# Optimization experiments

Measured on AMD Instinct MI355X. Metric: run time of the kernel, lower is better.

## Reference

```python
import jax, jax.numpy as jnp
import numpy as np

B, N, M, C = 64, 16384, 128, 1024  # batch, memory slots, memory unit size, ctrl dim
EPS = 1e-16


def _linear_params(k, fan_in, fan_out, gain=1.4):
    k1, k2 = jax.random.split(k)
    bound = gain * np.sqrt(6.0 / (fan_in + fan_out))  # xavier_uniform
    w = jax.random.uniform(k1, (fan_in, fan_out), jnp.float32, -bound, bound)
    b = jax.random.normal(k2, (fan_out,), jnp.float32) * 0.01
    return w, b


def setup_inputs() -> dict:
    key = jax.random.key(0)
    ks = jax.random.split(key, 10)
    ctrl_state = jax.random.normal(ks[0], (B, C), jnp.float32)
    pw = jax.random.uniform(ks[1], (B, N), jnp.float32)
    prev_weights = pw / pw.sum(axis=1, keepdims=True)
    memory = jax.random.normal(ks[2], (B, N, M), jnp.float32)
    key_w, key_b = _linear_params(ks[3], C, M)
    beta_w, beta_b = _linear_params(ks[4], C, 1)
    gate_w, gate_b = _linear_params(ks[5], C, 1)
    shift_w, shift_b = _linear_params(ks[6], C, 3)
    gamma_w, gamma_b = _linear_params(ks[7], C, 1)
    erase_w, erase_b = _linear_params(ks[8], C, M)
    add_w, add_b = _linear_params(ks[9], C, M)
    return dict(ctrl_state=ctrl_state, prev_weights=prev_weights, memory=memory,
                key_w=key_w, key_b=key_b, beta_w=beta_w, beta_b=beta_b,
                gate_w=gate_w, gate_b=gate_b, shift_w=shift_w, shift_b=shift_b,
                gamma_w=gamma_w, gamma_b=gamma_b, erase_w=erase_w, erase_b=erase_b,
                add_w=add_w, add_b=add_b)


def reference(ctrl_state, prev_weights, memory,
              key_w, key_b, beta_w, beta_b, gate_w, gate_b,
              shift_w, shift_b, gamma_w, gamma_b,
              erase_w, erase_b, add_w, add_b):
    # ---- parameter projections (7 small GEMMs + activations) ----
    k = jnp.tanh(ctrl_state @ key_w + key_b)                      # (B, M)
    beta = jax.nn.softplus(ctrl_state @ beta_w + beta_b)          # (B, 1)
    gate = jax.nn.sigmoid(ctrl_state @ gate_w + gate_b)           # (B, 1)
    shift = jax.nn.softmax(ctrl_state @ shift_w + shift_b, axis=1)  # (B, 3)
    gamma = 1.0 + jax.nn.softplus(ctrl_state @ gamma_w + gamma_b)   # (B, 1)
    # erase/add are computed by the head but unused in read ('r') mode
    _erase = jax.nn.sigmoid(ctrl_state @ erase_w + erase_b)
    _add = jnp.tanh(ctrl_state @ add_w + add_b)
    # ---- content addressing: cosine similarity then beta-sharpened softmax ----
    dots = jnp.einsum('bm,bnm->bn', k, memory)                    # (B, N)
    norms = jnp.linalg.norm(k, axis=1, keepdims=True) * jnp.linalg.norm(memory, axis=2)
    sim = dots / (norms + EPS)
    content_weights = jax.nn.softmax(beta * sim, axis=1)          # (B, N)
    # ---- gated interpolation ----
    w = gate * content_weights + (1.0 - gate) * prev_weights      # (B, N)
    # ---- circular convolutional shift (3-tap, max_shift=1) ----
    w = (shift[:, 0:1] * jnp.roll(w, 1, axis=1)
         + shift[:, 1:2] * w
         + shift[:, 2:3] * jnp.roll(w, -1, axis=1))
    # ---- sharpen ----
    wp = w ** gamma
    weights = wp / (wp.sum(axis=1, keepdims=True) + EPS)          # (B, N)
    # ---- read ----
    read_vec = jnp.einsum('bn,bnm->bm', weights, memory)          # (B, M)
    return weights, read_vec
```

## Files before the change

### kernel.cpp

```cpp
#include <hip/hip_runtime.h>
#include <math.h>

#define B_ 64
#define N_ 16384
#define M_ 128
#define C_ 1024
#define EPS_ 1e-16f

__device__ __forceinline__ float softplus_(float x) {
    return fmaxf(x, 0.f) + log1pf(expf(-fabsf(x)));
}

__global__ void proj_kernel(const float* __restrict__ ctrl,
                            const float* __restrict__ key_w, const float* __restrict__ key_b,
                            const float* __restrict__ beta_w, const float* __restrict__ beta_b,
                            const float* __restrict__ gate_w, const float* __restrict__ gate_b,
                            const float* __restrict__ shift_w, const float* __restrict__ shift_b,
                            const float* __restrict__ gamma_w, const float* __restrict__ gamma_b,
                            float* __restrict__ k_out, float* __restrict__ kn_out,
                            float* __restrict__ beta_out, float* __restrict__ gate_out,
                            float* __restrict__ gamma_out, float* __restrict__ shift_out)
{
    const int b = blockIdx.x;
    const int t = threadIdx.x;
    const float* c = ctrl + (size_t)b * C_;

    float acc = 0.f;
    for (int i = 0; i < C_; ++i) acc = fmaf(c[i], key_w[i * M_ + t], acc);
    float kv = tanhf(acc + key_b[t]);
    k_out[b * M_ + t] = kv;

    float p0 = 0, p1 = 0, p2 = 0, p3 = 0, p4 = 0, p5 = 0;
    for (int i = t; i < C_; i += 128) {
        float cv = c[i];
        p0 = fmaf(cv, beta_w[i],      p0);
        p1 = fmaf(cv, gate_w[i],      p1);
        p2 = fmaf(cv, gamma_w[i],     p2);
        p3 = fmaf(cv, shift_w[3*i+0], p3);
        p4 = fmaf(cv, shift_w[3*i+1], p4);
        p5 = fmaf(cv, shift_w[3*i+2], p5);
    }
    __shared__ float red[7][128];
    red[0][t] = p0; red[1][t] = p1; red[2][t] = p2;
    red[3][t] = p3; red[4][t] = p4; red[5][t] = p5;
    red[6][t] = kv * kv;
    __syncthreads();
    for (int s = 64; s > 0; s >>= 1) {
        if (t < s) {
            #pragma unroll
            for (int j = 0; j < 7; ++j) red[j][t] += red[j][t + s];
        }
        __syncthreads();
    }
    if (t == 0) {
        beta_out[b]  = softplus_(red[0][0] + beta_b[0]);
        gate_out[b]  = 1.f / (1.f + expf(-(red[1][0] + gate_b[0])));
        gamma_out[b] = 1.f + softplus_(red[2][0] + gamma_b[0]);
        float z0 = red[3][0] + shift_b[0];
        float z1 = red[4][0] + shift_b[1];
        float z2 = red[5][0] + shift_b[2];
        float mx = fmaxf(z0, fmaxf(z1, z2));
        float e0 = expf(z0 - mx), e1 = expf(z1 - mx), e2 = expf(z2 - mx);
        float inv = 1.f / (e0 + e1 + e2);
        shift_out[b*3+0] = e0 * inv;
        shift_out[b*3+1] = e1 * inv;
        shift_out[b*3+2] = e2 * inv;
        kn_out[b] = sqrtf(red[6][0]);
    }
}

#define ROWS_PER_CHUNK 1024
__global__ void content_kernel(const float* __restrict__ mem,
                               const float* __restrict__ k,
                               const float* __restrict__ kn,
                               const float* __restrict__ beta,
                               float* __restrict__ e_out,
                               float* __restrict__ sumE)
{
    const int b     = blockIdx.y;
    const int chunk = blockIdx.x;
    const int t     = threadIdx.x;
    const int wave  = t >> 6;
    const int lane  = t & 63;
    const int half  = lane >> 5;
    const int sub   = lane & 31;

    __shared__ float ks[M_];
    if (t < M_) ks[t] = k[b * M_ + t];
    __syncthreads();
    const float4 k4  = reinterpret_cast<const float4*>(ks)[sub];
    const float  knb = kn[b];
    const float  bet = beta[b];

    const float* memb = mem + (size_t)b * N_ * M_;
    const int rowbase = chunk * ROWS_PER_CHUNK + wave * 2 + half;

    float eacc = 0.f;
    #pragma unroll 4
    for (int i = 0; i < ROWS_PER_CHUNK / 8; ++i) {
        const int n = rowbase + i * 8;
        const float4 m4 = reinterpret_cast<const float4*>(memb + (size_t)n * M_)[sub];
        float d = m4.x*k4.x + m4.y*k4.y + m4.z*k4.z + m4.w*k4.w;
        float q = m4.x*m4.x + m4.y*m4.y + m4.z*m4.z + m4.w*m4.w;
        #pragma unroll
        for (int off = 1; off < 32; off <<= 1) {
            d += __shfl_xor(d, off, 64);
            q += __shfl_xor(q, off, 64);
        }
        if (sub == 0) {
            float sim = d / (knb * sqrtf(q) + EPS_);
            float ev  = expf(bet * sim);
            e_out[(size_t)b * N_ + n] = ev;
            eacc += ev;
        }
    }
    __shared__ float red[256];
    red[t] = eacc;
    __syncthreads();
    for (int s = 128; s > 0; s >>= 1) {
        if (t < s) red[t] += red[t + s];
        __syncthreads();
    }
    if (t == 0) atomicAdd(&sumE[b], red[0]);
}

__global__ void shiftpow_kernel(const float* __restrict__ e,
                                const float* __restrict__ prev,
                                const float* __restrict__ sumE,
                                const float* __restrict__ gate,
                                const float* __restrict__ shift,
                                const float* __restrict__ gamma,
                                float* __restrict__ wp_out,
                                float* __restrict__ sumWp)
{
    const int b = blockIdx.y;
    const int n = blockIdx.x * 256 + threadIdx.x;
    const float invE = 1.f / sumE[b];
    const float g    = gate[b];
    const float s0   = shift[b*3+0], s1 = shift[b*3+1], s2 = shift[b*3+2];
    const float gam  = gamma[b];
    const float* eb = e    + (size_t)b * N_;
    const float* pb = prev + (size_t)b * N_;

    const int nm = (n == 0)      ? N_ - 1 : n - 1;
    const int np = (n == N_ - 1) ? 0      : n + 1;
    float wm = g * eb[nm] * invE + (1.f - g) * pb[nm];
    float wc = g * eb[n]  * invE + (1.f - g) * pb[n];
    float wq = g * eb[np] * invE + (1.f - g) * pb[np];
    float wsft = s0 * wm + s1 * wc + s2 * wq;
    float wp = powf(wsft, gam);
    wp_out[(size_t)b * N_ + n] = wp;

    __shared__ float red[256];
    red[threadIdx.x] = wp;
    __syncthreads();
    for (int s = 128; s > 0; s >>= 1) {
        if (threadIdx.x < s) red[threadIdx.x] += red[threadIdx.x + s];
        __syncthreads();
    }
    if (threadIdx.x == 0) atomicAdd(&sumWp[b], red[0]);
}

__global__ void normalize_kernel(const float* __restrict__ wp,
                                 const float* __restrict__ sumWp,
                                 float* __restrict__ out_w)
{
    const int b = blockIdx.y;
    const int i = blockIdx.x * 256 + threadIdx.x;
    const float inv = 1.f / (sumWp[b] + EPS_);
    float4 v = reinterpret_cast<const float4*>(wp + (size_t)b * N_)[i];
    v.x *= inv; v.y *= inv; v.z *= inv; v.w *= inv;
    reinterpret_cast<float4*>(out_w + (size_t)b * N_)[i] = v;
}

__global__ void read_kernel(const float* __restrict__ mem,
                            const float* __restrict__ weights,
                            float* __restrict__ read_out)
{
    const int b     = blockIdx.y;
    const int chunk = blockIdx.x;
    const int t     = threadIdx.x;
    const int wave  = t >> 6;
    const int lane  = t & 63;
    const int half  = lane >> 5;
    const int sub   = lane & 31;

    __shared__ float wtile[ROWS_PER_CHUNK];
    for (int i = t; i < ROWS_PER_CHUNK; i += 256)
        wtile[i] = weights[(size_t)b * N_ + chunk * ROWS_PER_CHUNK + i];
    __syncthreads();

    const float* memb = mem + (size_t)b * N_ * M_;
    const int rowbase = chunk * ROWS_PER_CHUNK + wave * 2 + half;
    const int lbase   = wave * 2 + half;

    float4 acc = make_float4(0.f, 0.f, 0.f, 0.f);
    #pragma unroll 4
    for (int i = 0; i < ROWS_PER_CHUNK / 8; ++i) {
        const int n  = rowbase + i * 8;
        const float wn = wtile[lbase + i * 8];
        const float4 m4 = reinterpret_cast<const float4*>(memb + (size_t)n * M_)[sub];
        acc.x = fmaf(wn, m4.x, acc.x);
        acc.y = fmaf(wn, m4.y, acc.y);
        acc.z = fmaf(wn, m4.z, acc.z);
        acc.w = fmaf(wn, m4.w, acc.w);
    }
    __shared__ float red[8][32][4];
    const int g = wave * 2 + half;
    red[g][sub][0] = acc.x; red[g][sub][1] = acc.y;
    red[g][sub][2] = acc.z; red[g][sub][3] = acc.w;
    __syncthreads();
    if (t < M_) {
        const int m = t, s2 = m >> 2, c = m & 3;
        float s = 0.f;
        #pragma unroll
        for (int gg = 0; gg < 8; ++gg) s += red[gg][s2][c];
        atomicAdd(&read_out[b * M_ + m], s);
    }
}

extern "C" void kernel_launch(void* const* d_in, const int* in_sizes, int n_in,
                              void* d_out, int out_size, void* d_ws, size_t ws_size,
                              hipStream_t stream) {
    const float* ctrl    = (const float*)d_in[0];
    const float* prev_w  = (const float*)d_in[1];
    const float* memory  = (const float*)d_in[2];
    const float* key_w   = (const float*)d_in[3];
    const float* key_b   = (const float*)d_in[4];
    const float* beta_w  = (const float*)d_in[5];
    const float* beta_b  = (const float*)d_in[6];
    const float* gate_w  = (const float*)d_in[7];
    const float* gate_b  = (const float*)d_in[8];
    const float* shift_w = (const float*)d_in[9];
    const float* shift_b = (const float*)d_in[10];
    const float* gamma_w = (const float*)d_in[11];
    const float* gamma_b = (const float*)d_in[12];

    float* out   = (float*)d_out;
    float* ws    = (float*)d_ws;
    float* e     = ws;
    float* wp    = ws + (size_t)B_ * N_;
    float* kbuf  = ws + (size_t)2 * B_ * N_;
    float* kn    = kbuf  + B_ * M_;
    float* beta  = kn    + B_;
    float* gate  = beta  + B_;
    float* gamma = gate  + B_;
    float* shift = gamma + B_;
    float* sums  = shift + 3 * B_;
    float* sumE  = sums;
    float* sumWp = sums + B_;

    hipMemsetAsync(sums, 0, 2 * B_ * sizeof(float), stream);
    hipMemsetAsync(out + (size_t)B_ * N_, 0, B_ * M_ * sizeof(float), stream);

    proj_kernel<<<B_, 128, 0, stream>>>(ctrl, key_w, key_b, beta_w, beta_b,
                                        gate_w, gate_b, shift_w, shift_b,
                                        gamma_w, gamma_b,
                                        kbuf, kn, beta, gate, gamma, shift);

    content_kernel<<<dim3(N_ / ROWS_PER_CHUNK, B_), 256, 0, stream>>>(
        memory, kbuf, kn, beta, e, sumE);

    shiftpow_kernel<<<dim3(N_ / 256, B_), 256, 0, stream>>>(
        e, prev_w, sumE, gate, shift, gamma, wp, sumWp);

    normalize_kernel<<<dim3(N_ / 4 / 256, B_), 256, 0, stream>>>(wp, sumWp, out);

    read_kernel<<<dim3(N_ / ROWS_PER_CHUNK, B_), 256, 0, stream>>>(
        memory, out, out + (size_t)B_ * N_);
}
```

Baseline: 901.5 us.

## Fuse normalization into read kernel, widen proj block, restructure content row reduction

The normalize kernel is removed: the read kernel now scales the unnormalized powered weights by the inverse sum while loading its tile, and writes the normalized weights out. The content kernel assigns 8 lanes per memory row, each holding four float4s, so the cross-lane reduction drops from five shuffle steps to three. The projection kernel uses 256 threads and splits the key GEMM reduction across two halves. These changes aim to cut one launch and one full pass over the weights, and to reduce shuffle overhead in the bandwidth-bound content pass, at the cost of more registers per lane.

Result: slower. 1.034 ms (+14.7%).

```diff
diff --git a/kernel.cpp b/kernel.cpp
--- a/kernel.cpp
+++ b/kernel.cpp
@@ -6,6 +6,7 @@
 #define M_ 128
 #define C_ 1024
 #define EPS_ 1e-16f
+#define CHUNK_ 1024
 
 __device__ __forceinline__ float softplus_(float x) {
     return fmaxf(x, 0.f) + log1pf(expf(-fabsf(x)));
@@ -25,13 +26,24 @@
     const int t = threadIdx.x;
     const float* c = ctrl + (size_t)b * C_;
 
+    const int m    = t & 127;
+    const int half = t >> 7;
     float acc = 0.f;
-    for (int i = 0; i < C_; ++i) acc = fmaf(c[i], key_w[i * M_ + t], acc);
-    float kv = tanhf(acc + key_b[t]);
-    k_out[b * M_ + t] = kv;
+    const int i0 = half * (C_ / 2);
+    for (int i = i0; i < i0 + C_ / 2; ++i)
+        acc = fmaf(c[i], key_w[i * M_ + m], acc);
+
+    __shared__ float kred[256];
+    kred[t] = acc;
+    __syncthreads();
+    float kv = 0.f;
+    if (t < 128) {
+        kv = tanhf(kred[t] + kred[t + 128] + key_b[t]);
+        k_out[b * M_ + t] = kv;
+    }
 
     float p0 = 0, p1 = 0, p2 = 0, p3 = 0, p4 = 0, p5 = 0;
-    for (int i = t; i < C_; i += 128) {
+    for (int i = t; i < C_; i += 256) {
         float cv = c[i];
         p0 = fmaf(cv, beta_w[i],      p0);
         p1 = fmaf(cv, gate_w[i],      p1);
@@ -40,12 +52,12 @@
         p4 = fmaf(cv, shift_w[3*i+1], p4);
         p5 = fmaf(cv, shift_w[3*i+2], p5);
     }
-    __shared__ float red[7][128];
+    __shared__ float red[7][256];
     red[0][t] = p0; red[1][t] = p1; red[2][t] = p2;
     red[3][t] = p3; red[4][t] = p4; red[5][t] = p5;
-    red[6][t] = kv * kv;
-    __syncthreads();
-    for (int s = 64; s > 0; s >>= 1) {
+    red[6][t] = (t < 128) ? kv * kv : 0.f;
+    __syncthreads();
+    for (int s = 128; s > 0; s >>= 1) {
         if (t < s) {
             #pragma unroll
             for (int j = 0; j < 7; ++j) red[j][t] += red[j][t + s];
@@ -69,7 +81,6 @@
     }
 }
 
-#define ROWS_PER_CHUNK 1024
 __global__ void content_kernel(const float* __restrict__ mem,
                                const float* __restrict__ k,
                                const float* __restrict__ kn,
@@ -82,35 +93,42 @@
     const int t     = threadIdx.x;
     const int wave  = t >> 6;
     const int lane  = t & 63;
-    const int half  = lane >> 5;
-    const int sub   = lane & 31;
+    const int grp   = lane >> 3;
+    const int sub   = lane & 7;
 
     __shared__ float ks[M_];
     if (t < M_) ks[t] = k[b * M_ + t];
     __syncthreads();
-    const float4 k4  = reinterpret_cast<const float4*>(ks)[sub];
-    const float  knb = kn[b];
-    const float  bet = beta[b];
+    const float4* ks4 = reinterpret_cast<const float4*>(ks);
+    const float4 ka = ks4[sub], kb2 = ks4[sub + 8],
+                 kc = ks4[sub + 16], kd = ks4[sub + 24];
+    const float knb = kn[b];
+    const float bet = beta[b];
 
     const float* memb = mem + (size_t)b * N_ * M_;
-    const int rowbase = chunk * ROWS_PER_CHUNK + wave * 2 + half;
-
     float eacc = 0.f;
-    #pragma unroll 4
-    for (int i = 0; i < ROWS_PER_CHUNK / 8; ++i) {
-        const int n = rowbase + i * 8;
-        const float4 m4 = reinterpret_cast<const float4*>(memb + (size_t)n * M_)[sub];
-        float d = m4.x*k4.x + m4.y*k4.y + m4.z*k4.z + m4.w*k4.w;
-        float q = m4.x*m4.x + m4.y*m4.y + m4.z*m4.z + m4.w*m4.w;
-        #pragma unroll
-        for (int off = 1; off < 32; off <<= 1) {
-            d += __shfl_xor(d, off, 64);
-            q += __shfl_xor(q, off, 64);
-        }
+
+    #pragma unroll 2
+    for (int it = 0; it < CHUNK_ / 32; ++it) {
+        const int row = chunk * CHUNK_ + it * 32 + wave * 8 + grp;
+        const float4* rp = reinterpret_cast<const float4*>(memb + (size_t)row * M_);
+        const float4 m0 = rp[sub], m1 = rp[sub + 8],
+                     m2 = rp[sub + 16], m3 = rp[sub + 24];
+        float d = m0.x*ka.x  + m0.y*ka.y  + m0.z*ka.z  + m0.w*ka.w
+                + m1.x*kb2.x + m1.y*kb2.y + m1.z*kb2.z + m1.w*kb2.w
+                + m2.x*kc.x  + m2.y*kc.y  + m2.z*kc.z  + m2.w*kc.w
+                + m3.x*kd.x  + m3.y*kd.y  + m3.z*kd.z  + m3.w*kd.w;
+        float q = m0.x*m0.x + m0.y*m0.y + m0.z*m0.z + m0.w*m0.w
+                + m1.x*m1.x + m1.y*m1.y + m1.z*m1.z + m1.w*m1.w
+                + m2.x*m2.x + m2.y*m2.y + m2.z*m2.z + m2.w*m2.w
+                + m3.x*m3.x + m3.y*m3.y + m3.z*m3.z + m3.w*m3.w;
+        d += __shfl_xor(d, 1, 64); q += __shfl_xor(q, 1, 64);
+        d += __shfl_xor(d, 2, 64); q += __shfl_xor(q, 2, 64);
+        d += __shfl_xor(d, 4, 64); q += __shfl_xor(q, 4, 64);
         if (sub == 0) {
             float sim = d / (knb * sqrtf(q) + EPS_);
             float ev  = expf(bet * sim);
-            e_out[(size_t)b * N_ + n] = ev;
+            e_out[(size_t)b * N_ + row] = ev;
             eacc += ev;
         }
     }
@@ -161,20 +179,10 @@
     if (threadIdx.x == 0) atomicAdd(&sumWp[b], red[0]);
 }
 
-__global__ void normalize_kernel(const float* __restrict__ wp,
-                                 const float* __restrict__ sumWp,
-                                 float* __restrict__ out_w)
-{
-    const int b = blockIdx.y;
-    const int i = blockIdx.x * 256 + threadIdx.x;
-    const float inv = 1.f / (sumWp[b] + EPS_);
-    float4 v = reinterpret_cast<const float4*>(wp + (size_t)b * N_)[i];
-    v.x *= inv; v.y *= inv; v.z *= inv; v.w *= inv;
-    reinterpret_cast<float4*>(out_w + (size_t)b * N_)[i] = v;
-}
-
 __global__ void read_kernel(const float* __restrict__ mem,
-                            const float* __restrict__ weights,
+                            const float* __restrict__ wp,
+                            const float* __restrict__ sumWp,
+                            float* __restrict__ out_w,
                             float* __restrict__ read_out)
 {
     const int b     = blockIdx.y;
@@ -185,18 +193,25 @@
     const int half  = lane >> 5;
     const int sub   = lane & 31;
 
-    __shared__ float wtile[ROWS_PER_CHUNK];
-    for (int i = t; i < ROWS_PER_CHUNK; i += 256)
-        wtile[i] = weights[(size_t)b * N_ + chunk * ROWS_PER_CHUNK + i];
+    const float inv = 1.f / (sumWp[b] + EPS_);
+    const size_t base = (size_t)b * N_ + (size_t)chunk * CHUNK_;
+
+    __shared__ float wtile[CHUNK_];
+    {
+        float4 v = reinterpret_cast<const float4*>(wp + base)[t];
+        v.x *= inv; v.y *= inv; v.z *= inv; v.w *= inv;
+        reinterpret_cast<float4*>(wtile)[t] = v;
+        reinterpret_cast<float4*>(out_w + base)[t] = v;
+    }
     __syncthreads();
 
     const float* memb = mem + (size_t)b * N_ * M_;
-    const int rowbase = chunk * ROWS_PER_CHUNK + wave * 2 + half;
+    const int rowbase = chunk * CHUNK_ + wave * 2 + half;
     const int lbase   = wave * 2 + half;
 
     float4 acc = make_float4(0.f, 0.f, 0.f, 0.f);
     #pragma unroll 4
-    for (int i = 0; i < ROWS_PER_CHUNK / 8; ++i) {
+    for (int i = 0; i < CHUNK_ / 8; ++i) {
         const int n  = rowbase + i * 8;
         const float wn = wtile[lbase + i * 8];
         const float4 m4 = reinterpret_cast<const float4*>(memb + (size_t)n * M_)[sub];
@@ -211,11 +226,11 @@
     red[g][sub][2] = acc.z; red[g][sub][3] = acc.w;
     __syncthreads();
     if (t < M_) {
-        const int m = t, s2 = m >> 2, c = m & 3;
+        const int mm = t, s2 = mm >> 2, cc = mm & 3;
         float s = 0.f;
         #pragma unroll
-        for (int gg = 0; gg < 8; ++gg) s += red[gg][s2][c];
-        atomicAdd(&read_out[b * M_ + m], s);
+        for (int gg = 0; gg < 8; ++gg) s += red[gg][s2][cc];
+        atomicAdd(&read_out[b * M_ + mm], s);
     }
 }
 
@@ -253,19 +268,17 @@
     hipMemsetAsync(sums, 0, 2 * B_ * sizeof(float), stream);
     hipMemsetAsync(out + (size_t)B_ * N_, 0, B_ * M_ * sizeof(float), stream);
 
-    proj_kernel<<<B_, 128, 0, stream>>>(ctrl, key_w, key_b, beta_w, beta_b,
+    proj_kernel<<<B_, 256, 0, stream>>>(ctrl, key_w, key_b, beta_w, beta_b,
                                         gate_w, gate_b, shift_w, shift_b,
                                         gamma_w, gamma_b,
                                         kbuf, kn, beta, gate, gamma, shift);
 
-    content_kernel<<<dim3(N_ / ROWS_PER_CHUNK, B_), 256, 0, stream>>>(
+    content_kernel<<<dim3(N_ / CHUNK_, B_), 256, 0, stream>>>(
         memory, kbuf, kn, beta, e, sumE);
 
     shiftpow_kernel<<<dim3(N_ / 256, B_), 256, 0, stream>>>(
         e, prev_w, sumE, gate, shift, gamma, wp, sumWp);
 
-    normalize_kernel<<<dim3(N_ / 4 / 256, B_), 256, 0, stream>>>(wp, sumWp, out);
-
-    read_kernel<<<dim3(N_ / ROWS_PER_CHUNK, B_), 256, 0, stream>>>(
-        memory, out, out + (size_t)B_ * N_);
-}
+    read_kernel<<<dim3(N_ / CHUNK_, B_), 256, 0, stream>>>(
+        memory, wp, sumWp, out, out + (size_t)B_ * N_);
+}
```
